# Optimization experiments

Measured on AMD Instinct MI355X. Metric: run time of the kernel, lower is better.

The kernel has to match this reference:

```python
import jax, jax.numpy as jnp
import numpy as np

K = 9        # kernel size
M = 16       # m_max + 1 (angular frequencies, TensorCore-padded)
J = 8        # j_max + 1 (radial Bessel orders, TensorCore-padded)
CIN = 64
COUT = 64
N = 32
H = 64
W = 64


def setup_inputs() -> dict:
    key = jax.random.key(0)
    ks = jax.random.split(key, 6)
    fan_in = CIN * K * K
    x = jax.random.normal(ks[0], (N, CIN, H, W), dtype=jnp.float32)
    # Precomputed complex Bessel-Fourier transition matrix T (constant buffer),
    # shape (M, K*K, J), split into real/imag parts.
    T_real = jax.random.normal(ks[1], (M, K * K, J), dtype=jnp.float32) * 0.1
    T_imag = jax.random.normal(ks[2], (M, K * K, J), dtype=jnp.float32) * 0.1
    # Learnable spectral weights, He-style init scale sqrt(2/fan_in).
    w_scale = np.sqrt(2.0 / fan_in).astype(np.float32)
    w_r = jax.random.normal(ks[3], (M, J, CIN * COUT), dtype=jnp.float32) * w_scale
    w_i = jax.random.normal(ks[4], (M, J, CIN * COUT), dtype=jnp.float32) * w_scale
    # w_i for m=0 is zeroed in the original init
    w_i = w_i.at[0].set(0.0)
    bound = 1.0 / np.sqrt(fan_in)
    b = jax.random.uniform(ks[5], (COUT,), dtype=jnp.float32, minval=-bound, maxval=bound)
    return {"x": x, "T_real": T_real, "T_imag": T_imag, "w_r": w_r, "w_i": w_i, "b": b}


def reference(x, T_real, T_imag, w_r, w_i, b):
    # Complex matmul building the spatial filter bank:
    #   (M, K^2, J) @ (M, J, Cin*Cout) -> (M, K^2, Cin*Cout)
    wr = jnp.matmul(T_real, w_r) - jnp.matmul(T_imag, w_i)
    wi = jnp.matmul(T_real, w_i) + jnp.matmul(T_imag, w_r)
    # einops '[c] m (k1 k2) (b1 b2) -> (c m b2) b1 k1 k2'
    Wf = jnp.stack([wr, wi], axis=0).reshape(2, M, K, K, CIN, COUT)
    Wf = jnp.transpose(Wf, (0, 1, 5, 4, 2, 3)).reshape(2 * M * COUT, CIN, K, K)
    # conv2d, padding='same', stride=1
    y = jax.lax.conv_general_dilated(
        x, Wf, window_strides=(1, 1), padding='SAME',
        dimension_numbers=('NCHW', 'OIHW', 'NCHW'))
    # square (modulus pieces), then sum over (c, m): 'b (c m b1) w h -> b b1 w h'
    n, _, h, w = y.shape
    y = jnp.square(y).reshape(n, 2, M, COUT, h, w).sum(axis=(1, 2))
    # bias add; scale_inv=False -> take the single scale; activation=None
    return y + b[None, :, None, None]
```

## Files before the change

kernel.cpp:

```cpp
#include <hip/hip_runtime.h>
#include <stdint.h>


typedef unsigned short ushort_t;
typedef __attribute__((ext_vector_type(8))) short short8;
typedef __attribute__((ext_vector_type(4))) float float4v;

typedef const void __attribute__((address_space(1)))* gptr_t;
typedef void __attribute__((address_space(3)))* sptr_t;

__device__ __forceinline__ ushort_t f2bf(float f) {
    union { float f; uint32_t u; } v; v.f = f;
    uint32_t u = v.u;
    u += 0x7fffu + ((u >> 16) & 1u);
    return (ushort_t)(u >> 16);
}

__global__ __launch_bounds__(256) void pad_kernel(const float* __restrict__ x,
                                                  ushort_t* __restrict__ xp) {
    __shared__ float lds[64 * 65];
    const int hp  = blockIdx.x;
    const int b   = blockIdx.y;
    const int tid = threadIdx.x;
    const int h   = hp - 4;
    const bool hvalid = (h >= 0 && h < 64);
    if (hvalid) {
        #pragma unroll
        for (int it = 0; it < 16; ++it) {
            int idx = it * 256 + tid;
            int cin = idx >> 6, w = idx & 63;
            lds[w * 65 + cin] = x[((b * 64 + cin) * 64 + h) * 64 + w];
        }
    }
    __syncthreads();
    #pragma unroll
    for (int it = 0; it < 18; ++it) {
        int o = it * 256 + tid;
        int wp = o >> 6, cin = o & 63;
        int w = wp - 4;
        float val = (hvalid && w >= 0 && w < 64) ? lds[w * 65 + cin] : 0.0f;
        xp[((b * 72 + hp) * 72 + wp) * 64 + cin] = f2bf(val);
    }
}

__global__ __launch_bounds__(256) void wf_kernel(const float* __restrict__ Tr,
                                                 const float* __restrict__ Ti,
                                                 const float* __restrict__ wr,
                                                 const float* __restrict__ wi,
                                                 ushort_t* __restrict__ Wfb) {
    __shared__ float lds[64 * 65];
    const int g   = blockIdx.x;
    const int t   = blockIdx.y;
    const int part = g >> 4, m = g & 15;
    const int tid = threadIdx.x;
    #pragma unroll
    for (int it = 0; it < 16; ++it) {
        int cc = it * 256 + tid;
        float acc = 0.f;
        #pragma unroll
        for (int j = 0; j < 8; ++j) {
            float tr  = Tr[(m * 81 + t) * 8 + j];
            float ti  = Ti[(m * 81 + t) * 8 + j];
            float wrv = wr[(m * 8 + j) * 4096 + cc];
            float wiv = wi[(m * 8 + j) * 4096 + cc];
            acc += (part == 0) ? (tr * wrv - ti * wiv) : (tr * wiv + ti * wrv);
        }
        lds[(cc & 63) * 65 + (cc >> 6)] = acc;
    }
    __syncthreads();
    #pragma unroll
    for (int it = 0; it < 16; ++it) {
        int o = it * 256 + tid;
        int cout = o >> 6, cin = o & 63;
        Wfb[(t * 2048 + cout * 32 + g) * 64 + cin] = f2bf(lds[cout * 65 + cin]);
    }
}

__global__ __launch_bounds__(256, 2) void conv_kernel(const ushort_t* __restrict__ xp,
                                                      const ushort_t* __restrict__ Wfb,
                                                      const float* __restrict__ bias,
                                                      float* __restrict__ out) {
    __shared__ alignas(16) ushort_t As[5 * 72 * 64];
    __shared__ alignas(16) ushort_t Bs[2 * 128 * 64];

    const int bid = blockIdx.x;
    const int L   = (bid & 7) * 1024 + (bid >> 3);
    const int ct  = L >> 9;
    const int pt  = L & 511;
    const int b    = pt >> 4;
    const int h0   = (pt & 15) * 4;
    const int tid  = threadIdx.x;
    const int wv   = tid >> 6;
    const int lane = tid & 63;
    const int wrow = wv >> 1, wcol = wv & 1;
    const int quad = lane >> 4, lr = lane & 15;
    const int lsw  = ((lane & ~7) | ((lane ^ (lane >> 3)) & 7)) * 16;

    float4v acc[8][4];
    #pragma unroll
    for (int i = 0; i < 8; ++i)
        #pragma unroll
        for (int j = 0; j < 4; ++j) {
            float4v z = {0.f, 0.f, 0.f, 0.f};
            acc[i][j] = z;
        }

    const char* xpb  = (const char*)xp;
    const char* wfb0 = (const char*)Wfb + (size_t)(ct * 128) * 128;

    auto stageA = [&](int row, int slot) {
        char* dstb = (char*)As + slot * 9216;
        const char* gb = xpb + (size_t)(b * 72 + h0 + row) * 9216 + (size_t)lsw;
        __builtin_amdgcn_global_load_lds((gptr_t)(gb + (size_t)wv * 1024),
            (sptr_t)(dstb + wv * 1024), 16, 0, 0);
        __builtin_amdgcn_global_load_lds((gptr_t)(gb + (size_t)(wv + 4) * 1024),
            (sptr_t)(dstb + (wv + 4) * 1024), 16, 0, 0);
        if (wv == 0)
            __builtin_amdgcn_global_load_lds((gptr_t)(gb + (size_t)8 * 1024),
                (sptr_t)(dstb + 8 * 1024), 16, 0, 0);
    };
    auto stageB = [&](int t) {
        const char* base = wfb0 + (size_t)t * 262144;
        char* dst = (char*)Bs + (t & 1) * 16384;
        #pragma unroll
        for (int k2 = 0; k2 < 4; ++k2) {
            const int c2 = wv * 4 + k2;
            __builtin_amdgcn_global_load_lds((gptr_t)(base + (size_t)c2 * 1024 + (size_t)lsw),
                (sptr_t)(dst + c2 * 1024), 16, 0, 0);
        }
    };

    stageA(0, 0); stageA(1, 1); stageA(2, 2); stageA(3, 3);
    stageB(0);

    const int wrowu = __builtin_amdgcn_readfirstlane(wrow);
    int s4  = 4;
    int rs0 = wrowu * 2;
    int rs1 = rs0 + 1;

    const int bkey = lr & 7;
    for (int dy = 0; dy < 9; ++dy) {
        const int ab0 = rs0 * 72;
        const int ab1 = rs1 * 72;
        for (int dx = 0; dx < 9; ++dx) {
            const int t = dy * 9 + dx;
            __syncthreads();
            if (t < 80) stageB(t + 1);
            if (dx == 0 && dy < 8) stageA(dy + 4, s4);

            const ushort_t* Bp = Bs + (t & 1) * 8192;
            const int akey = (lr + dx) & 7;
            const int pxb  = lr + dx;
            #pragma unroll
            for (int kk = 0; kk < 2; ++kk) {
                short8 a[8], bb[4];
                const int aslot = ((kk * 4 + quad) ^ akey) * 8;
                const int bslot = ((kk * 4 + quad) ^ bkey) * 8;
                #pragma unroll
                for (int j = 0; j < 4; ++j)
                    bb[j] = *(const short8*)&Bp[(wcol * 64 + j * 16 + lr) * 64 + bslot];
                #pragma unroll
                for (int i = 0; i < 8; ++i) {
                    const int ab = (i >> 2) ? ab1 : ab0;
                    a[i] = *(const short8*)&As[(ab + pxb + (i & 3) * 16) * 64 + aslot];
                }
                #pragma unroll
                for (int i = 0; i < 8; ++i)
                    #pragma unroll
                    for (int j = 0; j < 4; ++j)
                        acc[i][j] = __builtin_amdgcn_mfma_f32_16x16x32_bf16(
                            a[i], bb[j], acc[i][j], 0, 0, 0);
            }
        }
        s4  = (s4  == 4) ? 0 : s4  + 1;
        rs0 = (rs0 == 4) ? 0 : rs0 + 1;
        rs1 = (rs1 == 4) ? 0 : rs1 + 1;
    }

    const int c0 = ct * 4 + wcol * 2;
    const float b0 = bias[c0], b1 = bias[c0 + 1];
    #pragma unroll
    for (int i = 0; i < 8; ++i) {
        #pragma unroll
        for (int reg = 0; reg < 4; ++reg) {
            float v0 = acc[i][0][reg] * acc[i][0][reg] + acc[i][1][reg] * acc[i][1][reg];
            float v1 = acc[i][2][reg] * acc[i][2][reg] + acc[i][3][reg] * acc[i][3][reg];
            #pragma unroll
            for (int off = 1; off <= 8; off <<= 1) {
                v0 += __shfl_xor(v0, off, 64);
                v1 += __shfl_xor(v1, off, 64);
            }
            if (lr == 0) {
                const int w = (i & 3) * 16 + quad * 4 + reg;
                const int h = h0 + wrow * 2 + (i >> 2);
                out[((b * 64 + c0    ) * 64 + h) * 64 + w] = v0 + b0;
                out[((b * 64 + c0 + 1) * 64 + h) * 64 + w] = v1 + b1;
            }
        }
    }
}

extern "C" void kernel_launch(void* const* d_in, const int* in_sizes, int n_in,
                              void* d_out, int out_size, void* d_ws, size_t ws_size,
                              hipStream_t stream) {
    const float* x    = (const float*)d_in[0];
    const float* Tr   = (const float*)d_in[1];
    const float* Ti   = (const float*)d_in[2];
    const float* wr   = (const float*)d_in[3];
    const float* wi   = (const float*)d_in[4];
    const float* bias = (const float*)d_in[5];
    float* out = (float*)d_out;

    ushort_t* xp  = (ushort_t*)d_ws;
    ushort_t* Wfb = (ushort_t*)((char*)d_ws + 21233664);

    pad_kernel<<<dim3(72, 32), 256, 0, stream>>>(x, xp);
    wf_kernel<<<dim3(32, 81), 256, 0, stream>>>(Tr, Ti, wr, wi, Wfb);
    conv_kernel<<<dim3(8192), 256, 0, stream>>>(xp, Wfb, bias, out);
}
```

Before: 1.954 ms.

## Load conv weight fragments directly into registers instead of staging through LDS

Drops the double-buffered LDS staging of the filter tile. Each lane now loads its B fragments straight from global memory into registers, prefetching the next tap while the current MFMAs run. This removes the per-tap __syncthreads, leaving a single barrier per kernel row when the input row is staged. The trade is extra global/L2 traffic, since each wave now loads its own weights with no cross-wave sharing, plus more register pressure; waves_per_eu is pinned at 2.

Result: slower. 2.549 ms (+30.5%).

```diff
diff --git a/kernel.cpp b/kernel.cpp
--- a/kernel.cpp
+++ b/kernel.cpp
@@ -76,12 +76,12 @@
     }
 }
 
-__global__ __launch_bounds__(256, 2) void conv_kernel(const ushort_t* __restrict__ xp,
-                                                      const ushort_t* __restrict__ Wfb,
-                                                      const float* __restrict__ bias,
-                                                      float* __restrict__ out) {
+__global__ __launch_bounds__(256, 2) __attribute__((amdgpu_waves_per_eu(2, 2)))
+void conv_kernel(const ushort_t* __restrict__ xp,
+                 const ushort_t* __restrict__ Wfb,
+                 const float* __restrict__ bias,
+                 float* __restrict__ out) {
     __shared__ alignas(16) ushort_t As[5 * 72 * 64];
-    __shared__ alignas(16) ushort_t Bs[2 * 128 * 64];
 
     const int bid = blockIdx.x;
     const int L   = (bid & 7) * 1024 + (bid >> 3);
@@ -105,8 +105,9 @@
             acc[i][j] = z;
         }
 
-    const char* xpb  = (const char*)xp;
-    const char* wfb0 = (const char*)Wfb + (size_t)(ct * 128) * 128;
+    const char* xpb = (const char*)xp;
+    const char* tb = (const char*)Wfb
+        + (size_t)(ct * 128 + wcol * 64 + lr) * 128 + (size_t)quad * 16;
 
     auto stageA = [&](int row, int slot) {
         char* dstb = (char*)As + slot * 9216;
@@ -119,46 +120,38 @@
             __builtin_amdgcn_global_load_lds((gptr_t)(gb + (size_t)8 * 1024),
                 (sptr_t)(dstb + 8 * 1024), 16, 0, 0);
     };
-    auto stageB = [&](int t) {
-        const char* base = wfb0 + (size_t)t * 262144;
-        char* dst = (char*)Bs + (t & 1) * 16384;
-        #pragma unroll
-        for (int k2 = 0; k2 < 4; ++k2) {
-            const int c2 = wv * 4 + k2;
-            __builtin_amdgcn_global_load_lds((gptr_t)(base + (size_t)c2 * 1024 + (size_t)lsw),
-                (sptr_t)(dst + c2 * 1024), 16, 0, 0);
-        }
-    };
 
     stageA(0, 0); stageA(1, 1); stageA(2, 2); stageA(3, 3);
-    stageB(0);
+
+    short8 bc[4], bn[4];
+    bc[0] = *(const short8*)(tb);
+    bc[1] = *(const short8*)(tb + 2048);
+    bc[2] = *(const short8*)(tb + 4096);
+    bc[3] = *(const short8*)(tb + 6144);
 
     const int wrowu = __builtin_amdgcn_readfirstlane(wrow);
     int s4  = 4;
     int rs0 = wrowu * 2;
     int rs1 = rs0 + 1;
 
-    const int bkey = lr & 7;
     for (int dy = 0; dy < 9; ++dy) {
+        __syncthreads();
+        if (dy < 8) stageA(dy + 4, s4);
         const int ab0 = rs0 * 72;
         const int ab1 = rs1 * 72;
         for (int dx = 0; dx < 9; ++dx) {
             const int t = dy * 9 + dx;
-            __syncthreads();
-            if (t < 80) stageB(t + 1);
-            if (dx == 0 && dy < 8) stageA(dy + 4, s4);
-
-            const ushort_t* Bp = Bs + (t & 1) * 8192;
             const int akey = (lr + dx) & 7;
             const int pxb  = lr + dx;
-            #pragma unroll
-            for (int kk = 0; kk < 2; ++kk) {
-                short8 a[8], bb[4];
-                const int aslot = ((kk * 4 + quad) ^ akey) * 8;
-                const int bslot = ((kk * 4 + quad) ^ bkey) * 8;
-                #pragma unroll
-                for (int j = 0; j < 4; ++j)
-                    bb[j] = *(const short8*)&Bp[(wcol * 64 + j * 16 + lr) * 64 + bslot];
+
+            bn[0] = *(const short8*)(tb + 64);
+            bn[1] = *(const short8*)(tb + 2048 + 64);
+            bn[2] = *(const short8*)(tb + 4096 + 64);
+            bn[3] = *(const short8*)(tb + 6144 + 64);
+
+            {
+                const int aslot = (quad ^ akey) * 8;
+                short8 a[8];
                 #pragma unroll
                 for (int i = 0; i < 8; ++i) {
                     const int ab = (i >> 2) ? ab1 : ab0;
@@ -169,8 +162,34 @@
                     #pragma unroll
                     for (int j = 0; j < 4; ++j)
                         acc[i][j] = __builtin_amdgcn_mfma_f32_16x16x32_bf16(
-                            a[i], bb[j], acc[i][j], 0, 0, 0);
-            }
+                            a[i], bc[j], acc[i][j], 0, 0, 0);
+            }
+
+            {
+                const char* tbn = tb + (t < 80 ? 262144 : 0);
+                bc[0] = *(const short8*)(tbn);
+                bc[1] = *(const short8*)(tbn + 2048);
+                bc[2] = *(const short8*)(tbn + 4096);
+                bc[3] = *(const short8*)(tbn + 6144);
+            }
+
+            {
+                const int aslot = ((4 + quad) ^ akey) * 8;
+                short8 a[8];
+                #pragma unroll
+                for (int i = 0; i < 8; ++i) {
+                    const int ab = (i >> 2) ? ab1 : ab0;
+                    a[i] = *(const short8*)&As[(ab + pxb + (i & 3) * 16) * 64 + aslot];
+                }
+                #pragma unroll
+                for (int i = 0; i < 8; ++i)
+                    #pragma unroll
+                    for (int j = 0; j < 4; ++j)
+                        acc[i][j] = __builtin_amdgcn_mfma_f32_16x16x32_bf16(
+                            a[i], bn[j], acc[i][j], 0, 0, 0);
+            }
+
+            tb += 262144;
         }
         s4  = (s4  == 4) ? 0 : s4  + 1;
         rs0 = (rs0 == 4) ? 0 : rs0 + 1;
```
